# Kernel tuning notes

Hardware: AMD Instinct MI355X
Metric: run time of the kernel (lower is better)

## Reference

```python
import jax, jax.numpy as jnp
import numpy as np

B, S, D, H, L = 8, 4096, 512, 512, 2


def log_g(x):
    # log of g(x) where g(x) = x + 0.5 for x >= 0 else sigmoid(x)
    return jnp.where(x >= 0, jnp.log(jax.nn.relu(x) + 0.5), -jax.nn.softplus(-x))


def g(x):
    return jnp.where(x >= 0, x + 0.5, jax.nn.sigmoid(x))


def mingru_layer(x, h0, wz, bz, wh, bh):
    """Log-space parallel-scan minGRU layer.
    x: (B,S,Din), h0: (B,1,H) positive (already g-activated).
    wz,wh: (H,Din); bz,bh: (H,). Returns full hidden sequence (B,S,H)."""
    k = jnp.einsum('bsd,hd->bsh', x, wz) + bz          # gate pre-activation
    log_z = -jax.nn.softplus(-k)                        # log sigmoid(k)
    log_coeffs = -jax.nn.softplus(k)                    # log(1 - sigmoid(k))
    log_h_tilde = log_g(jnp.einsum('bsd,hd->bsh', x, wh) + bh)
    log_values = log_z + log_h_tilde                    # log(z * h_tilde)
    log_h0 = jnp.log(h0)                                # (B,1,H)
    # Heinsen associative scan in log space
    a_star = jnp.cumsum(
        jnp.concatenate([jnp.zeros_like(log_h0), log_coeffs], axis=1), axis=1)  # (B,S+1,H)
    log_vals = jnp.concatenate([log_h0, log_values], axis=1)                     # (B,S+1,H)
    log_h = a_star + jax.lax.cumlogsumexp(log_vals - a_star, axis=1)
    return jnp.exp(log_h)[:, 1:]                        # (B,S,H)


def setup_inputs() -> dict:
    key = jax.random.key(0)
    ks = jax.random.split(key, 1 + 4 * L)
    x = jax.random.normal(ks[0], (B, S, D), dtype=jnp.float32)
    inp = {'x': x}
    dims_in = [D] + [H] * (L - 1)
    i = 1
    for l in range(L):
        din = dims_in[l]
        stdv = 1.0 / np.sqrt(din)
        inp[f'wz{l}'] = jax.random.uniform(ks[i], (H, din), minval=-stdv, maxval=stdv); i += 1
        inp[f'bz{l}'] = jax.random.uniform(ks[i], (H,), minval=-stdv, maxval=stdv); i += 1
        inp[f'wh{l}'] = jax.random.uniform(ks[i], (H, din), minval=-stdv, maxval=stdv); i += 1
        inp[f'bh{l}'] = jax.random.uniform(ks[i], (H,), minval=-stdv, maxval=stdv); i += 1
    return inp


def reference(x, wz0, bz0, wh0, bh0, wz1, bz1, wh1, bh1):
    # h is None -> h0 = g(zeros) = 0.5 for every layer
    h0 = jnp.full((B, 1, H), 0.5, dtype=x.dtype)
    params = [(wz0, bz0, wh0, bh0), (wz1, bz1, wh1, bh1)]
    inp = x
    finals = []
    for (wz, bz, wh, bh) in params:
        out = mingru_layer(inp, h0, wz, bz, wh, bh)
        finals.append(out[:, -1:])
        inp = out  # Identity layer transform, no residual, dropout=0
    return out, jnp.stack(finals)  # (B,S,H), (L,B,1,H)
```

## Files before the change

kernel.cpp:

```cpp
#include <hip/hip_runtime.h>
#include <math.h>

#define BB 8
#define SS 4096
#define DD 512
#define HH 512
#define MM (BB*SS)

constexpr int TCH = 64;
constexpr int NC  = SS / TCH;
constexpr int BH  = BB * HH;

constexpr int BM = 128;
constexpr int BN = 64;
constexpr int BK = 64;

typedef short  short8  __attribute__((ext_vector_type(8)));
typedef float  float4v __attribute__((ext_vector_type(4)));

__device__ inline unsigned short f2bf(float f) {
    union { float f; unsigned u; } v; v.f = f;
    unsigned r = v.u + 0x7FFF + ((v.u >> 16) & 1);
    return (unsigned short)(r >> 16);
}
__device__ inline float bf_lo(unsigned u) {
    union { unsigned u; float f; } x; x.u = u << 16; return x.f;
}
__device__ inline float bf_hi(unsigned u) {
    union { unsigned u; float f; } x; x.u = u & 0xffff0000u; return x.f;
}
__device__ inline float fast_rcp(float x) {
    return __builtin_amdgcn_rcpf(x);
}

__device__ inline void async_copy16(const void* g, void* l) {
    __builtin_amdgcn_global_load_lds(
        (const __attribute__((address_space(1))) void*)g,
        (__attribute__((address_space(3))) void*)l, 16, 0, 0);
}

__global__ __launch_bounds__(256)
void conv_all(const float* __restrict__ x,
              const float* __restrict__ w0, const float* __restrict__ w1,
              const float* __restrict__ w2, const float* __restrict__ w3,
              short* __restrict__ Xbf, short* __restrict__ Wbf)
{
    constexpr int XBLK = MM * DD / 8 / 256;
    constexpr int WBLK = HH * DD / 8 / 256;
    const int bid = blockIdx.x;
    const float* src; short* dst; size_t base;
    if (bid < XBLK) {
        src = x; dst = Xbf;
        base = ((size_t)bid * 256 + threadIdx.x) * 8;
    } else {
        const int idx  = bid - XBLK;
        const int wsel = idx / WBLK;
        src = (wsel == 0) ? w0 : (wsel == 1) ? w1 : (wsel == 2) ? w2 : w3;
        dst = Wbf + (size_t)wsel * HH * DD;
        base = ((size_t)(idx % WBLK) * 256 + threadIdx.x) * 8;
    }
    float4 a = *(const float4*)(src + base);
    float4 b = *(const float4*)(src + base + 4);
    short8 r;
    r[0] = f2bf(a.x); r[1] = f2bf(a.y); r[2] = f2bf(a.z); r[3] = f2bf(a.w);
    r[4] = f2bf(b.x); r[5] = f2bf(b.y); r[6] = f2bf(b.z); r[7] = f2bf(b.w);
    *(short8*)(dst + base) = r;
}

__global__ __launch_bounds__(256)
void gemm_gate_mfma(const short* __restrict__ Xg, const short* __restrict__ Wz,
                    const float* __restrict__ bz, const short* __restrict__ Wh,
                    const float* __restrict__ bh, unsigned* __restrict__ AV,
                    float2* __restrict__ cAV)
{
    __shared__ char smem[65536];
    short*    lds    = (short*)smem;
    unsigned* lds_av = (unsigned*)smem;
    constexpr int BUFS = 16384;
    constexpr int ZOFF = BM * BK;
    constexpr int HOFF = ZOFF + BN * BK;
    constexpr int NIT  = DD / BK;

    const int t    = threadIdx.x;
    const int wave = t >> 6;
    const int lane = t & 63;
    const int col16 = lane & 15;
    const int quad  = lane >> 4;
    const int wm = wave >> 1;
    const int wn = wave & 1;
    const int m0 = blockIdx.x * BM;
    const int n0 = blockIdx.y * BN;

    float4v accz[4][2], acch[4][2];
    #pragma unroll
    for (int i = 0; i < 4; ++i)
        #pragma unroll
        for (int j = 0; j < 2; ++j) {
            accz[i][j] = (float4v){0.f, 0.f, 0.f, 0.f};
            acch[i][j] = (float4v){0.f, 0.f, 0.f, 0.f};
        }

    const int lr  = lane >> 3;
    const int lcs = (((lane & 7) ^ lr) * 8);

    auto stage = [&](int buf, int k0) {
        short* L = lds + buf * BUFS;
        #pragma unroll
        for (int i = 0; i < 4; ++i) {
            const int r0 = wave * 32 + i * 8;
            async_copy16(Xg + (size_t)(m0 + r0 + lr) * DD + k0 + lcs,
                         &L[r0 * BK]);
        }
        #pragma unroll
        for (int i = 0; i < 2; ++i) {
            const int r0 = wave * 16 + i * 8;
            async_copy16(Wz + (size_t)(n0 + r0 + lr) * DD + k0 + lcs,
                         &L[ZOFF + r0 * BK]);
            async_copy16(Wh + (size_t)(n0 + r0 + lr) * DD + k0 + lcs,
                         &L[HOFF + r0 * BK]);
        }
    };

    stage(0, 0);
    asm volatile("s_waitcnt vmcnt(0)" ::: "memory");
    __builtin_amdgcn_s_barrier();
    asm volatile("" ::: "memory");

    const int swz = (col16 & 7) * 8;

    #pragma unroll
    for (int it = 0; it < NIT; ++it) {
        if (it + 1 < NIT) stage((it + 1) & 1, (it + 1) * BK);

        const short* L = lds + (it & 1) * BUFS;
        #pragma unroll
        for (int kk = 0; kk < 2; ++kk) {
            const int ko = (kk * 32 + quad * 8) ^ swz;
            short8 af[4], bzf[2], bhf[2];
            #pragma unroll
            for (int mi = 0; mi < 4; ++mi)
                af[mi] = *(const short8*)&L[(wm*64 + mi*16 + col16) * BK + ko];
            #pragma unroll
            for (int nj = 0; nj < 2; ++nj) {
                bzf[nj] = *(const short8*)&L[ZOFF + (wn*32 + nj*16 + col16) * BK + ko];
                bhf[nj] = *(const short8*)&L[HOFF + (wn*32 + nj*16 + col16) * BK + ko];
            }
            #pragma unroll
            for (int mi = 0; mi < 4; ++mi)
                #pragma unroll
                for (int nj = 0; nj < 2; ++nj) {
                    accz[mi][nj] = __builtin_amdgcn_mfma_f32_16x16x32_bf16(af[mi], bzf[nj], accz[mi][nj], 0, 0, 0);
                    acch[mi][nj] = __builtin_amdgcn_mfma_f32_16x16x32_bf16(af[mi], bhf[nj], acch[mi][nj], 0, 0, 0);
                }
        }
        asm volatile("s_waitcnt vmcnt(0) lgkmcnt(0)" ::: "memory");
        __builtin_amdgcn_s_barrier();
        asm volatile("" ::: "memory");
    }

    #pragma unroll
    for (int nj = 0; nj < 2; ++nj) {
        const int ln = wn*32 + nj*16 + col16;
        const int n  = n0 + ln;
        const float bzn = bz[n], bhn = bh[n];
        #pragma unroll
        for (int mi = 0; mi < 4; ++mi) {
            const int lmb = wm*64 + mi*16 + quad*4;
            #pragma unroll
            for (int reg = 0; reg < 4; ++reg) {
                const float kz = accz[mi][nj][reg] + bzn;
                const float kh = acch[mi][nj][reg] + bhn;
                const float a  = fast_rcp(1.0f + __expf(kz));
                const float sn = fast_rcp(1.0f + __expf(-kh));
                const float ht = (kh >= 0.0f) ? (kh + 0.5f) : sn;
                const float v  = (1.0f - a) * ht;
                lds_av[(lmb + reg) * 64 + ln] = ((unsigned)f2bf(v) << 16) | f2bf(a);
            }
        }
    }
    __syncthreads();

    {
        const int row0 = t >> 4;
        const int col  = (t & 15) * 4;
        #pragma unroll
        for (int i = 0; i < 8; ++i) {
            const int row = row0 + i * 16;
            const uint4 u = *(const uint4*)&lds_av[row * 64 + col];
            *(uint4*)&AV[(size_t)(m0 + row) * HH + n0 + col] = u;
        }
    }

    {
        const int task = t >> 1;
        const int hf   = t & 1;
        const int c    = task >> 6;
        const int ln   = task & 63;
        float prod = 1.0f, hl = 0.0f;
        #pragma unroll 8
        for (int s = 0; s < TCH / 2; ++s) {
            const unsigned u = lds_av[(c * TCH + hf * 32 + s) * 64 + ln];
            const float a = bf_lo(u), v = bf_hi(u);
            hl   = fmaf(a, hl, v);
            prod *= a;
        }
        const float pA = __shfl_xor(prod, 1);
        const float pV = __shfl_xor(hl, 1);
        if (hf == 0) {
            const int b  = m0 >> 12;
            const int cg = ((m0 & 4095) >> 6) + c;
            cAV[(size_t)cg * BH + b * HH + (n0 + ln)] =
                make_float2(prod * pA, fmaf(pA, hl, pV));
        }
    }
}

__global__ __launch_bounds__(256)
void chunk_prefix(const float2* __restrict__ cAV, float* __restrict__ H0)
{
    const int ch = blockIdx.x * 256 + threadIdx.x;
    float h = 0.5f;
    #pragma unroll
    for (int c = 0; c < NC; ++c) {
        H0[(size_t)c * BH + ch] = h;
        const float2 s = cAV[(size_t)c * BH + ch];
        h = fmaf(s.x, h, s.y);
    }
}

__global__ __launch_bounds__(256)
void scan_apply_f32(const unsigned* __restrict__ AV,
                    const float* __restrict__ H0,
                    float* __restrict__ out, float* __restrict__ finals)
{
    const int h = blockIdx.x * 256 + threadIdx.x;
    const int b = blockIdx.y;
    const int c = blockIdx.z;
    const int ch = b * HH + h;
    float hcur = H0[(size_t)c * BH + ch];
    size_t base = ((size_t)(b * SS + c * TCH)) * HH + h;
    #pragma unroll
    for (int tt = 0; tt < TCH; ++tt) {
        const unsigned u = AV[base];
        hcur = fmaf(bf_lo(u), hcur, bf_hi(u));
        __builtin_nontemporal_store(hcur, &out[base]);
        base += HH;
    }
    if (c == NC - 1) finals[ch] = hcur;
}

__global__ __launch_bounds__(256)
void scan_apply_bf16(const unsigned* __restrict__ AV,
                     const float* __restrict__ H0,
                     short* __restrict__ out, float* __restrict__ finals)
{
    const int h = blockIdx.x * 256 + threadIdx.x;
    const int b = blockIdx.y;
    const int c = blockIdx.z;
    const int ch = b * HH + h;
    float hcur = H0[(size_t)c * BH + ch];
    size_t base = ((size_t)(b * SS + c * TCH)) * HH + h;
    #pragma unroll
    for (int tt = 0; tt < TCH; ++tt) {
        const unsigned u = AV[base];
        hcur = fmaf(bf_lo(u), hcur, bf_hi(u));
        out[base] = (short)f2bf(hcur);
        base += HH;
    }
    if (c == NC - 1) finals[ch] = hcur;
}

extern "C" void kernel_launch(void* const* d_in, const int* in_sizes, int n_in,
                              void* d_out, int out_size, void* d_ws, size_t ws_size,
                              hipStream_t stream)
{
    const float* x   = (const float*)d_in[0];
    const float* wz0 = (const float*)d_in[1];
    const float* bz0 = (const float*)d_in[2];
    const float* wh0 = (const float*)d_in[3];
    const float* bh0 = (const float*)d_in[4];
    const float* wz1 = (const float*)d_in[5];
    const float* bz1 = (const float*)d_in[6];
    const float* wh1 = (const float*)d_in[7];
    const float* bh1 = (const float*)d_in[8];

    float* out    = (float*)d_out;
    float* finals = out + (size_t)MM * HH;

    unsigned* AV  = (unsigned*)d_ws;
    short* Xbf    = (short*)(AV + (size_t)MM * HH);
    short* Wbf    = Xbf + (size_t)MM * DD;
    float2* cAV   = (float2*)(Wbf + (size_t)4 * HH * DD);
    float* H0     = (float*)(cAV + (size_t)NC * BH);

    short* Wz0 = Wbf;
    short* Wh0 = Wbf + (size_t)1 * HH * DD;
    short* Wz1 = Wbf + (size_t)2 * HH * DD;
    short* Wh1 = Wbf + (size_t)3 * HH * DD;

    const dim3 gg(MM / BM, HH / BN);
    const dim3 gs(HH / 256, BB, NC);

    conv_all<<<MM * DD / 8 / 256 + 4 * (HH * DD / 8 / 256), 256, 0, stream>>>(
        x, wz0, wh0, wz1, wh1, Xbf, Wbf);

    gemm_gate_mfma <<<gg, 256, 0, stream>>>(Xbf, Wz0, bz0, Wh0, bh0, AV, cAV);
    chunk_prefix   <<<BH / 256, 256, 0, stream>>>(cAV, H0);
    scan_apply_bf16<<<gs, 256, 0, stream>>>(AV, H0, Xbf, finals);

    gemm_gate_mfma <<<gg, 256, 0, stream>>>(Xbf, Wz1, bz1, Wh1, bh1, AV, cAV);
    chunk_prefix   <<<BH / 256, 256, 0, stream>>>(cAV, H0);
    scan_apply_f32 <<<gs, 256, 0, stream>>>(AV, H0, out, finals + BH);
}
```

Measured before the change: 290.5 us.

## Store gate/value pairs chunk-major and compute chunk summaries in registers

The GEMM epilogue no longer stages the packed (a, v) pairs through LDS. Each lane writes its four consecutive-timestep values as one uint4 into a chunk-major AV layout, then builds chunk summaries with register scans combined through cross-lane shuffles. The scan-apply kernels read that layout with 16-byte vector loads along time instead of strided scalar loads. The aim is to remove the LDS round-trip, a barrier, and uncoalesced scalar AV reads, at the cost of strided 16-byte global stores in the epilogue and per-thread strided vector reads in the scan.

```diff
diff --git a/kernel.cpp b/kernel.cpp
--- a/kernel.cpp
+++ b/kernel.cpp
@@ -74,8 +74,7 @@
                     float2* __restrict__ cAV)
 {
     __shared__ char smem[65536];
-    short*    lds    = (short*)smem;
-    unsigned* lds_av = (unsigned*)smem;
+    short* lds = (short*)smem;
     constexpr int BUFS = 16384;
     constexpr int ZOFF = BM * BK;
     constexpr int HOFF = ZOFF + BN * BK;
@@ -158,59 +157,52 @@
         asm volatile("" ::: "memory");
     }
 
-    #pragma unroll
-    for (int nj = 0; nj < 2; ++nj) {
-        const int ln = wn*32 + nj*16 + col16;
-        const int n  = n0 + ln;
-        const float bzn = bz[n], bhn = bh[n];
-        #pragma unroll
-        for (int mi = 0; mi < 4; ++mi) {
-            const int lmb = wm*64 + mi*16 + quad*4;
+    {
+        const int b  = m0 >> 12;
+        const int cw = ((m0 & 4095) >> 6) + wm;
+        const size_t cg = (size_t)(m0 >> 6) + wm;
+
+        #pragma unroll
+        for (int nj = 0; nj < 2; ++nj) {
+            const int ln = wn*32 + nj*16 + col16;
+            const int n  = n0 + ln;
+            const float bzn = bz[n], bhn = bh[n];
+            float cA = 1.0f, cV = 0.0f;
             #pragma unroll
-            for (int reg = 0; reg < 4; ++reg) {
-                const float kz = accz[mi][nj][reg] + bzn;
-                const float kh = acch[mi][nj][reg] + bhn;
-                const float a  = fast_rcp(1.0f + __expf(kz));
-                const float sn = fast_rcp(1.0f + __expf(-kh));
-                const float ht = (kh >= 0.0f) ? (kh + 0.5f) : sn;
-                const float v  = (1.0f - a) * ht;
-                lds_av[(lmb + reg) * 64 + ln] = ((unsigned)f2bf(v) << 16) | f2bf(a);
+            for (int mi = 0; mi < 4; ++mi) {
+                unsigned pk[4];
+                float sA = 1.0f, sV = 0.0f;
+                #pragma unroll
+                for (int reg = 0; reg < 4; ++reg) {
+                    const float kz = accz[mi][nj][reg] + bzn;
+                    const float kh = acch[mi][nj][reg] + bhn;
+                    const float a  = fast_rcp(1.0f + __expf(kz));
+                    const float sn = fast_rcp(1.0f + __expf(-kh));
+                    const float ht = (kh >= 0.0f) ? (kh + 0.5f) : sn;
+                    const float v  = (1.0f - a) * ht;
+                    const unsigned u = ((unsigned)f2bf(v) << 16) | f2bf(a);
+                    pk[reg] = u;
+                    const float ar = bf_lo(u), vr = bf_hi(u);
+                    sV = fmaf(ar, sV, vr);
+                    sA *= ar;
+                }
+                *(uint4*)&AV[(cg * HH + n) * TCH + mi*16 + quad*4] =
+                    make_uint4(pk[0], pk[1], pk[2], pk[3]);
+                {
+                    float oA = __shfl_xor(sA, 16), oV = __shfl_xor(sV, 16);
+                    float lA = (quad & 1) ? oA : sA, lV = (quad & 1) ? oV : sV;
+                    float rA = (quad & 1) ? sA : oA, rV = (quad & 1) ? sV : oV;
+                    sA = lA * rA; sV = fmaf(rA, lV, rV);
+                    oA = __shfl_xor(sA, 32); oV = __shfl_xor(sV, 32);
+                    lA = (quad & 2) ? oA : sA; lV = (quad & 2) ? oV : sV;
+                    rA = (quad & 2) ? sA : oA; rV = (quad & 2) ? sV : oV;
+                    sA = lA * rA; sV = fmaf(rA, lV, rV);
+                }
+                cV = fmaf(sA, cV, sV);
+                cA = cA * sA;
             }
-        }
-    }
-    __syncthreads();
-
-    {
-        const int row0 = t >> 4;
-        const int col  = (t & 15) * 4;
-        #pragma unroll
-        for (int i = 0; i < 8; ++i) {
-            const int row = row0 + i * 16;
-            const uint4 u = *(const uint4*)&lds_av[row * 64 + col];
-            *(uint4*)&AV[(size_t)(m0 + row) * HH + n0 + col] = u;
-        }
-    }
-
-    {
-        const int task = t >> 1;
-        const int hf   = t & 1;
-        const int c    = task >> 6;
-        const int ln   = task & 63;
-        float prod = 1.0f, hl = 0.0f;
-        #pragma unroll 8
-        for (int s = 0; s < TCH / 2; ++s) {
-            const unsigned u = lds_av[(c * TCH + hf * 32 + s) * 64 + ln];
-            const float a = bf_lo(u), v = bf_hi(u);
-            hl   = fmaf(a, hl, v);
-            prod *= a;
-        }
-        const float pA = __shfl_xor(prod, 1);
-        const float pV = __shfl_xor(hl, 1);
-        if (hf == 0) {
-            const int b  = m0 >> 12;
-            const int cg = ((m0 & 4095) >> 6) + c;
-            cAV[(size_t)cg * BH + b * HH + (n0 + ln)] =
-                make_float2(prod * pA, fmaf(pA, hl, pV));
+            if (quad == 0)
+                cAV[(size_t)cw * BH + b * HH + n] = make_float2(cA, cV);
         }
     }
 }
@@ -238,13 +230,20 @@
     const int c = blockIdx.z;
     const int ch = b * HH + h;
     float hcur = H0[(size_t)c * BH + ch];
+    const uint4* src = (const uint4*)(AV + ((size_t)(b * NC + c) * HH + h) * TCH);
     size_t base = ((size_t)(b * SS + c * TCH)) * HH + h;
     #pragma unroll
-    for (int tt = 0; tt < TCH; ++tt) {
-        const unsigned u = AV[base];
-        hcur = fmaf(bf_lo(u), hcur, bf_hi(u));
+    for (int j = 0; j < TCH / 4; ++j) {
+        const uint4 u = src[j];
+        hcur = fmaf(bf_lo(u.x), hcur, bf_hi(u.x));
         __builtin_nontemporal_store(hcur, &out[base]);
-        base += HH;
+        hcur = fmaf(bf_lo(u.y), hcur, bf_hi(u.y));
+        __builtin_nontemporal_store(hcur, &out[base + HH]);
+        hcur = fmaf(bf_lo(u.z), hcur, bf_hi(u.z));
+        __builtin_nontemporal_store(hcur, &out[base + 2 * HH]);
+        hcur = fmaf(bf_lo(u.w), hcur, bf_hi(u.w));
+        __builtin_nontemporal_store(hcur, &out[base + 3 * HH]);
+        base += 4 * HH;
     }
     if (c == NC - 1) finals[ch] = hcur;
 }
@@ -259,13 +258,20 @@
     const int c = blockIdx.z;
     const int ch = b * HH + h;
     float hcur = H0[(size_t)c * BH + ch];
+    const uint4* src = (const uint4*)(AV + ((size_t)(b * NC + c) * HH + h) * TCH);
     size_t base = ((size_t)(b * SS + c * TCH)) * HH + h;
     #pragma unroll
-    for (int tt = 0; tt < TCH; ++tt) {
-        const unsigned u = AV[base];
-        hcur = fmaf(bf_lo(u), hcur, bf_hi(u));
+    for (int j = 0; j < TCH / 4; ++j) {
+        const uint4 u = src[j];
+        hcur = fmaf(bf_lo(u.x), hcur, bf_hi(u.x));
         out[base] = (short)f2bf(hcur);
-        base += HH;
+        hcur = fmaf(bf_lo(u.y), hcur, bf_hi(u.y));
+        out[base + HH] = (short)f2bf(hcur);
+        hcur = fmaf(bf_lo(u.z), hcur, bf_hi(u.z));
+        out[base + 2 * HH] = (short)f2bf(hcur);
+        hcur = fmaf(bf_lo(u.w), hcur, bf_hi(u.w));
+        out[base + 3 * HH] = (short)f2bf(hcur);
+        base += 4 * HH;
     }
     if (c == NC - 1) finals[ch] = hcur;
 }
```

After: 293.3 us. No clear change (+0.9%).
